# Optimization experiments

Hardware: AMD Instinct MI355X
Metric: run time of the kernel (lower is better)

Reference implementation:

```python
import jax, jax.numpy as jnp
import numpy as np

N = 50000
E = 1600000
NEG_SLOPE = 0.2
EPS = 1e-16


def gat_conv(x, src, dst, W, att_src, att_dst, bias):
    # x: [N, F_in]; W: [F_in, H*C]; att_*: [H, C]; bias: [H*C]
    H, C = att_src.shape
    h = (x @ W).reshape(-1, H, C)               # [N, H, C]
    a_src = jnp.sum(h * att_src[None], axis=-1)  # [N, H]
    a_dst = jnp.sum(h * att_dst[None], axis=-1)  # [N, H]
    e = a_src[src] + a_dst[dst]                  # [E, H]
    e = jnp.where(e > 0, e, NEG_SLOPE * e)       # leaky_relu
    # segment softmax over incoming edges of each destination node
    m = jax.ops.segment_max(e, dst, num_segments=N)          # [N, H]
    ex = jnp.exp(e - m[dst])                                  # [E, H]
    s = jax.ops.segment_sum(ex, dst, num_segments=N)          # [N, H]
    alpha = ex / (s[dst] + EPS)                               # [E, H]
    out = jax.ops.segment_sum(h[src] * alpha[:, :, None], dst, num_segments=N)  # [N, H, C]
    return out.reshape(-1, H * C) + bias


def setup_inputs() -> dict:
    key = jax.random.key(0)
    ks = jax.random.split(key, 12)
    x = jax.random.normal(ks[0], (N, 128), dtype=jnp.float32)
    edge_index = jax.random.randint(ks[1], (2, E), 0, N, dtype=jnp.int64)
    W1 = jax.random.normal(ks[2], (128, 128), dtype=jnp.float32) * 0.1
    att_src1 = jax.random.normal(ks[3], (4, 32), dtype=jnp.float32) * 0.1
    att_dst1 = jax.random.normal(ks[4], (4, 32), dtype=jnp.float32) * 0.1
    bias1 = jax.random.normal(ks[5], (128,), dtype=jnp.float32) * 0.1
    W2 = jax.random.normal(ks[6], (128, 64), dtype=jnp.float32) * 0.1
    att_src2 = jax.random.normal(ks[7], (1, 64), dtype=jnp.float32) * 0.1
    att_dst2 = jax.random.normal(ks[8], (1, 64), dtype=jnp.float32) * 0.1
    bias2 = jax.random.normal(ks[9], (64,), dtype=jnp.float32) * 0.1
    return {"x": x, "edge_index": edge_index, "W1": W1, "att_src1": att_src1,
            "att_dst1": att_dst1, "bias1": bias1, "W2": W2, "att_src2": att_src2,
            "att_dst2": att_dst2, "bias2": bias2}


def reference(x, edge_index, W1, att_src1, att_dst1, bias1, W2, att_src2, att_dst2, bias2):
    # GATConv adds self loops by default
    loops = jnp.arange(N, dtype=edge_index.dtype)
    src = jnp.concatenate([edge_index[0], loops])
    dst = jnp.concatenate([edge_index[1], loops])
    # eval mode: dropouts are identity
    h = gat_conv(x, src, dst, W1, att_src1, att_dst1, bias1)
    h = jax.nn.elu(h)
    out = gat_conv(h, src, dst, W2, att_src2, att_dst2, bias2)
    return out
```

## Files before the change

### kernel.cpp

```cpp
#include <hip/hip_runtime.h>
#include <hip/hip_fp16.h>
#include <math.h>


#define NB_BUCKETS 256
#define BCAP 16384

typedef _Float16 half8 __attribute__((ext_vector_type(8)));
typedef float    floatx4 __attribute__((ext_vector_type(4)));

__device__ __forceinline__ unsigned short f2h_bits(float f) {
    return __half_as_ushort(__float2half(f));
}
__device__ __forceinline__ float h2f_lo(unsigned int u) {
    return __half2float(__ushort_as_half((unsigned short)(u & 0xFFFFu)));
}
__device__ __forceinline__ float h2f_hi(unsigned int u) {
    return __half2float(__ushort_as_half((unsigned short)(u >> 16)));
}

__global__ __launch_bounds__(256) void splitA_kernel(const int* __restrict__ eidx,
        unsigned int* __restrict__ tmp, int* __restrict__ coarse_fill,
        int E, int etot, int nb)
{
    __shared__ int hist[NB_BUCKETS];
    __shared__ int gb[NB_BUCKETS];
    __shared__ int cnt2[NB_BUCKETS];
    int t = threadIdx.x;
    if (t < nb) { hist[t] = 0; cnt2[t] = 0; }
    __syncthreads();

    unsigned int val[16];
    int bkt[16];
    int base = blockIdx.x * 4096;
    #pragma unroll
    for (int i = 0; i < 16; i++) {
        int idx = base + i * 256 + t;
        if (idx < etot) {
            unsigned int s, d;
            if (idx < E) { s = (unsigned int)eidx[idx]; d = (unsigned int)eidx[E + idx]; }
            else         { s = (unsigned int)(idx - E); d = s; }
            val[i] = (d << 16) | s;
            bkt[i] = (int)(d >> 8);
            atomicAdd(&hist[bkt[i]], 1);
        } else {
            bkt[i] = -1;
        }
    }
    __syncthreads();
    if (t < nb) {
        int n = hist[t];
        gb[t] = (n > 0) ? atomicAdd(&coarse_fill[t], n) : 0;
    }
    __syncthreads();
    #pragma unroll
    for (int i = 0; i < 16; i++) {
        if (bkt[i] >= 0) {
            int loc = atomicAdd(&cnt2[bkt[i]], 1);
            tmp[(size_t)bkt[i] * BCAP + gb[bkt[i]] + loc] = val[i];
        }
    }
}

__global__ __launch_bounds__(256) void scanB_kernel(const int* __restrict__ coarse_fill,
        int* __restrict__ bucket_base, int nb, int N_, int etot, int* __restrict__ rowp)
{
    __shared__ int sd[256];
    int t = threadIdx.x;
    int c = (t < nb) ? coarse_fill[t] : 0;
    sd[t] = c;
    __syncthreads();
    for (int off = 1; off < 256; off <<= 1) {
        int y = (t >= off) ? sd[t - off] : 0;
        __syncthreads();
        sd[t] += y;
        __syncthreads();
    }
    if (t < nb) bucket_base[t] = sd[t] - c;
    if (t == 0) rowp[N_] = etot;
}

__global__ __launch_bounds__(1024) void passB_kernel(const unsigned int* __restrict__ tmp,
        const int* __restrict__ coarse_fill, const int* __restrict__ bucket_base,
        int* __restrict__ col, int* __restrict__ rowp, int N_)
{
    __shared__ int hist2[256];
    __shared__ int scn[256];
    __shared__ int off2[256];
    int b = blockIdx.x;
    int t = threadIdx.x;
    int n = coarse_fill[b];
    int base = bucket_base[b];
    const unsigned int* seg = tmp + (size_t)b * BCAP;

    if (t < 256) hist2[t] = 0;
    __syncthreads();
    for (int i = t; i < n; i += 1024) {
        unsigned int v = seg[i];
        atomicAdd(&hist2[(v >> 16) & 255], 1);
    }
    __syncthreads();
    int myc = (t < 256) ? hist2[t] : 0;
    if (t < 256) scn[t] = myc;
    __syncthreads();
    for (int off = 1; off < 256; off <<= 1) {
        int y = 0;
        if (t < 256 && t >= off) y = scn[t - off];
        __syncthreads();
        if (t < 256) scn[t] += y;
        __syncthreads();
    }
    if (t < 256) {
        int excl = scn[t] - myc;
        off2[t] = excl;
        int node = b * 256 + t;
        if (node <= N_) rowp[node] = base + excl;
    }
    __syncthreads();
    for (int i = t; i < n; i += 1024) {
        unsigned int v = seg[i];
        int bin = (v >> 16) & 255;
        int loc = atomicAdd(&off2[bin], 1);
        col[base + loc] = (int)(v & 0xFFFFu);
    }
}

template<int NT, int H, bool AF16>
__global__ __launch_bounds__(256) void gemm_attn_kernel(
        const void* __restrict__ Xv, const float* __restrict__ W,
        const float* __restrict__ att_s, const float* __restrict__ att_d,
        unsigned short* __restrict__ Hf16, float* __restrict__ as_,
        float* __restrict__ ad_, int M)
{
    constexpr int D = NT * 16;
    constexpr int C = D / H;
    __shared__ _Float16 Bs[NT * 4 * 64 * 8];

    int t = threadIdx.x;
    for (int idx = t; idx < 128 * D; idx += 256) {
        int k = idx / D;
        int n = idx - k * D;
        int nt = n >> 4, ks = k >> 5;
        int lane = (((k >> 3) & 3) << 4) | (n & 15);
        int j = k & 7;
        Bs[(((nt * 4 + ks) * 64 + lane) << 3) + j] = (_Float16)W[idx];
    }
    __syncthreads();

    int lane = t & 63;
    int wv = t >> 6;
    int quad = lane >> 4, colL = lane & 15;
    int row0 = blockIdx.x * 64 + wv * 16;

    int arow = row0 + colL; if (arow > M - 1) arow = M - 1;
    half8 afrag[4];
    if constexpr (AF16) {
        const unsigned short* Xh = (const unsigned short*)Xv;
        #pragma unroll
        for (int ks = 0; ks < 4; ks++)
            afrag[ks] = *(const half8*)(const void*)(Xh + (size_t)arow * 128 + ks * 32 + quad * 8);
    } else {
        const float* Xf = (const float*)Xv;
        #pragma unroll
        for (int ks = 0; ks < 4; ks++) {
            const float* pa = Xf + (size_t)arow * 128 + ks * 32 + quad * 8;
            float4 a0 = *(const float4*)pa;
            float4 a1 = *(const float4*)(pa + 4);
            half8 f;
            f[0] = (_Float16)a0.x; f[1] = (_Float16)a0.y;
            f[2] = (_Float16)a0.z; f[3] = (_Float16)a0.w;
            f[4] = (_Float16)a1.x; f[5] = (_Float16)a1.y;
            f[6] = (_Float16)a1.z; f[7] = (_Float16)a1.w;
            afrag[ks] = f;
        }
    }

    floatx4 acc[NT];
    #pragma unroll
    for (int nt = 0; nt < NT; nt++) {
        floatx4 c = {0.f, 0.f, 0.f, 0.f};
        #pragma unroll
        for (int ks = 0; ks < 4; ks++) {
            half8 b = *(half8*)(void*)&Bs[(((nt * 4 + ks) * 64 + lane) << 3)];
            c = __builtin_amdgcn_mfma_f32_16x16x32_f16(afrag[ks], b, c, 0, 0, 0);
        }
        acc[nt] = c;
    }

    float atts[NT], attd[NT];
    #pragma unroll
    for (int nt = 0; nt < NT; nt++) {
        int ch = nt * 16 + colL;
        atts[nt] = att_s[ch];
        attd[nt] = att_d[ch];
    }
    float ps[H][4], pd[H][4];
    #pragma unroll
    for (int h = 0; h < H; h++)
        #pragma unroll
        for (int r = 0; r < 4; r++) { ps[h][r] = 0.f; pd[h][r] = 0.f; }
    #pragma unroll
    for (int nt = 0; nt < NT; nt++) {
        int h = (nt * 16) / C;
        #pragma unroll
        for (int r = 0; r < 4; r++) {
            ps[h][r] += acc[nt][r] * atts[nt];
            pd[h][r] += acc[nt][r] * attd[nt];
        }
    }
    #pragma unroll
    for (int h = 0; h < H; h++)
        #pragma unroll
        for (int r = 0; r < 4; r++)
            #pragma unroll
            for (int off = 1; off < 16; off <<= 1) {
                ps[h][r] += __shfl_xor(ps[h][r], off);
                pd[h][r] += __shfl_xor(pd[h][r], off);
            }
    if (colL < H) {
        #pragma unroll
        for (int r = 0; r < 4; r++) {
            int row = row0 + quad * 4 + r;
            if (row < M) {
                float vs, vd;
                if constexpr (H == 4) {
                    vs = colL == 0 ? ps[0][r] : colL == 1 ? ps[1][r] : colL == 2 ? ps[2][r] : ps[3][r];
                    vd = colL == 0 ? pd[0][r] : colL == 1 ? pd[1][r] : colL == 2 ? pd[2][r] : pd[3][r];
                } else {
                    vs = ps[0][r]; vd = pd[0][r];
                }
                as_[(size_t)row * H + colL] = vs;
                ad_[(size_t)row * H + colL] = vd;
            }
        }
    }

    #pragma unroll
    for (int r = 0; r < 4; r++) {
        int row = row0 + quad * 4 + r;
        if (row < M) {
            #pragma unroll
            for (int nt = 0; nt < NT; nt++)
                Hf16[(size_t)row * D + nt * 16 + colL] = f2h_bits(acc[nt][r]);
        }
    }
}

template<int H, int C, bool ELU_, bool OUTF16>
__global__ __launch_bounds__(256) void aggregate_fused(
        const int* __restrict__ row_ptr, const int* __restrict__ col_src,
        const unsigned short* __restrict__ payload, const float* __restrict__ asv,
        const float* __restrict__ adv, const float* __restrict__ bias,
        void* __restrict__ outv, int nnodes)
{
    constexpr int D = H * C;
    constexpr int CPL = 8;
    constexpr int LPE = D / CPL;
    constexpr int EPI = 64 / LPE;
    __shared__ float2 exs[4][H][65];
    int wave = threadIdx.x >> 6, lane = threadIdx.x & 63;
    int node = blockIdx.x * 4 + wave;
    if (node >= nnodes) return;
    int start = row_ptr[node];
    int deg   = row_ptr[node + 1] - start;
    int li  = lane & (LPE - 1);
    int sub = lane / LPE;
    int myh = (li * CPL) / C;
    int lane_off = li * 16;

    float adh[H];
    #pragma unroll
    for (int h = 0; h < H; h++) adh[h] = adv[(size_t)node * H + h];

    float m[H];
    #pragma unroll
    for (int h = 0; h < H; h++) m[h] = -3.0e38f;
    float acc[CPL];
    #pragma unroll
    for (int k = 0; k < CPL; k++) acc[k] = 0.f;
    float sacc = 0.f;
    const char* pb = (const char*)payload;

    for (int c0 = 0; c0 < deg; c0 += 64) {
        int cnt = deg - c0; if (cnt > 64) cnt = 64;
        int idx = c0 + lane;
        int svec = 0;
        float e[H];
        if (idx < deg) {
            svec = col_src[start + idx];
            if constexpr (H == 4) {
                float4 av = *(const float4*)(asv + (size_t)svec * 4);
                float t0 = av.x + adh[0], t1 = av.y + adh[1];
                float t2 = av.z + adh[2], t3 = av.w + adh[3];
                e[0] = fmaxf(t0, 0.2f * t0); e[1] = fmaxf(t1, 0.2f * t1);
                e[2] = fmaxf(t2, 0.2f * t2); e[3] = fmaxf(t3, 0.2f * t3);
            } else {
                float tt = asv[svec] + adh[0];
                e[0] = fmaxf(tt, 0.2f * tt);
            }
        } else {
            #pragma unroll
            for (int h = 0; h < H; h++) e[h] = -3.0e38f;
        }
        float nm[H];
        #pragma unroll
        for (int h = 0; h < H; h++) {
            float v = e[h];
            #pragma unroll
            for (int off = 32; off >= 1; off >>= 1)
                v = fmaxf(v, __shfl_xor(v, off));
            nm[h] = fmaxf(m[h], v);
        }
        float sc = __expf(m[myh] - nm[myh]);
        sacc *= sc;
        #pragma unroll
        for (int k = 0; k < CPL; k++) acc[k] *= sc;
        #pragma unroll
        for (int h = 0; h < H; h++) m[h] = nm[h];

        unsigned int boff = (unsigned int)svec * (unsigned int)(D * 2);
        float boff_f = __uint_as_float(boff);
        #pragma unroll
        for (int h = 0; h < H; h++) {
            float ex = (idx < deg) ? __expf(e[h] - m[h]) : 0.f;
            exs[wave][h][lane] = make_float2(ex, boff_f);
        }

        int iters = (cnt + EPI - 1) / EPI;
        #pragma unroll 2
        for (int it = 0; it < iters; it++) {
            int el = it * EPI + sub;
            float2 v = exs[wave][myh][el];
            float exj = v.x;
            unsigned int off = __float_as_uint(v.y);
            uint4 hv = *(const uint4*)(const void*)(pb + off + lane_off);
            sacc += exj;
            acc[0] = fmaf(h2f_lo(hv.x), exj, acc[0]);
            acc[1] = fmaf(h2f_hi(hv.x), exj, acc[1]);
            acc[2] = fmaf(h2f_lo(hv.y), exj, acc[2]);
            acc[3] = fmaf(h2f_hi(hv.y), exj, acc[3]);
            acc[4] = fmaf(h2f_lo(hv.z), exj, acc[4]);
            acc[5] = fmaf(h2f_hi(hv.z), exj, acc[5]);
            acc[6] = fmaf(h2f_lo(hv.w), exj, acc[6]);
            acc[7] = fmaf(h2f_hi(hv.w), exj, acc[7]);
        }
    }

    #pragma unroll
    for (int off = LPE; off < 64; off <<= 1) {
        sacc += __shfl_xor(sacc, off);
        #pragma unroll
        for (int k = 0; k < CPL; k++) acc[k] += __shfl_xor(acc[k], off);
    }
    if (sub == 0) {
        float inv = 1.f / (sacc + 1e-16f);
        int ch = li * CPL;
        float r[CPL];
        #pragma unroll
        for (int k = 0; k < CPL; k++) {
            r[k] = acc[k] * inv + bias[ch + k];
            if (ELU_) r[k] = r[k] > 0.f ? r[k] : (__expf(r[k]) - 1.f);
        }
        if constexpr (OUTF16) {
            unsigned short* o = (unsigned short*)outv;
            unsigned int w0 = (unsigned int)f2h_bits(r[0]) | ((unsigned int)f2h_bits(r[1]) << 16);
            unsigned int w1 = (unsigned int)f2h_bits(r[2]) | ((unsigned int)f2h_bits(r[3]) << 16);
            unsigned int w2 = (unsigned int)f2h_bits(r[4]) | ((unsigned int)f2h_bits(r[5]) << 16);
            unsigned int w3 = (unsigned int)f2h_bits(r[6]) | ((unsigned int)f2h_bits(r[7]) << 16);
            uint4 q = { w0, w1, w2, w3 };
            *(uint4*)(void*)(o + (size_t)node * D + ch) = q;
        } else {
            float* o = (float*)outv;
            float4 w0 = { r[0], r[1], r[2], r[3] };
            float4 w1 = { r[4], r[5], r[6], r[7] };
            *(float4*)(o + (size_t)node * D + ch) = w0;
            *(float4*)(o + (size_t)node * D + ch + 4) = w1;
        }
    }
}

extern "C" void kernel_launch(void* const* d_in, const int* in_sizes, int n_in,
                              void* d_out, int out_size, void* d_ws, size_t ws_size,
                              hipStream_t stream)
{
    const float* x        = (const float*)d_in[0];
    const int*   eidx     = (const int*)  d_in[1];
    const float* W1       = (const float*)d_in[2];
    const float* att_src1 = (const float*)d_in[3];
    const float* att_dst1 = (const float*)d_in[4];
    const float* bias1    = (const float*)d_in[5];
    const float* W2       = (const float*)d_in[6];
    const float* att_src2 = (const float*)d_in[7];
    const float* att_dst2 = (const float*)d_in[8];
    const float* bias2    = (const float*)d_in[9];
    float* out = (float*)d_out;

    const int N_ = in_sizes[0] / 128;
    const int E_ = in_sizes[1] / 2;
    const int ET = E_ + N_;
    const int NB = (N_ + 255) / 256;

    char* p = (char*)d_ws;
    auto alloc = [&](size_t bytes) {
        void* r = (void*)p;
        p += ((bytes + 255) / 256) * 256;
        return r;
    };
    int* rowp  = (int*)alloc((size_t)(N_ + 1) * 4);
    int* cfill = (int*)alloc((size_t)NB_BUCKETS * 4);
    int* bbase = (int*)alloc((size_t)NB_BUCKETS * 4);
    int* colidx = (int*)alloc((size_t)ET * 4);
    unsigned int*   tmp   = (unsigned int*)alloc((size_t)NB_BUCKETS * BCAP * 4);
    unsigned short* h1f16 = (unsigned short*)tmp;
    unsigned short* hx16  = (unsigned short*)alloc((size_t)N_ * 128 * 2);
    unsigned short* h2f16 = (unsigned short*)alloc((size_t)N_ * 64 * 2);
    float* as1 = (float*)alloc((size_t)N_ * 4 * 4);
    float* ad1 = (float*)alloc((size_t)N_ * 4 * 4);
    float* as2 = (float*)alloc((size_t)N_ * 4);
    float* ad2 = (float*)alloc((size_t)N_ * 4);
    (void)ws_size; (void)n_in; (void)out_size;

    hipMemsetAsync(cfill, 0, (size_t)NB_BUCKETS * 4, stream);
    splitA_kernel<<<(ET + 4095) / 4096, 256, 0, stream>>>(eidx, tmp, cfill, E_, ET, NB);
    scanB_kernel<<<1, 256, 0, stream>>>(cfill, bbase, NB, N_, ET, rowp);
    passB_kernel<<<NB, 1024, 0, stream>>>(tmp, cfill, bbase, colidx, rowp, N_);

    gemm_attn_kernel<8, 4, false><<<(N_ + 63) / 64, 256, 0, stream>>>(
        x, W1, att_src1, att_dst1, h1f16, as1, ad1, N_);
    aggregate_fused<4, 32, true, true><<<(N_ + 3) / 4, 256, 0, stream>>>(
        rowp, colidx, h1f16, as1, ad1, bias1, hx16, N_);

    gemm_attn_kernel<4, 1, true><<<(N_ + 63) / 64, 256, 0, stream>>>(
        hx16, W2, att_src2, att_dst2, h2f16, as2, ad2, N_);
    aggregate_fused<1, 64, false, false><<<(N_ + 3) / 4, 256, 0, stream>>>(
        rowp, colidx, h2f16, as2, ad2, bias2, out, N_);
}
```

Before: 245.5 us.

## Merge CSR build with first GEMM, fold scan into passB, split aggregation channels

Runs the first GEMM+attention blocks and the edge-bucketing blocks in one launch so they share the device. The single-block scan kernel is folded into passB, where each block recomputes the bucket prefix sum itself. The aggregation kernels now split channels into two halves across separate blocks, which doubles block count and halves per-wave payload width but recomputes softmax weights twice per edge. h1 gets its own buffer instead of aliasing the tmp buffer, because the tmp buckets are now written concurrently.

After: 271.3 us. +10.5%, slower.

```diff
diff --git a/kernel.cpp b/kernel.cpp
--- a/kernel.cpp
+++ b/kernel.cpp
@@ -19,7 +19,7 @@
     return __half2float(__ushort_as_half((unsigned short)(u >> 16)));
 }
 
-__global__ __launch_bounds__(256) void splitA_kernel(const int* __restrict__ eidx,
+__device__ void splitA_body(int bx, const int* __restrict__ eidx,
         unsigned int* __restrict__ tmp, int* __restrict__ coarse_fill,
         int E, int etot, int nb)
 {
@@ -32,7 +32,7 @@
 
     unsigned int val[16];
     int bkt[16];
-    int base = blockIdx.x * 4096;
+    int base = bx * 4096;
     #pragma unroll
     for (int i = 0; i < 16; i++) {
         int idx = base + i * 256 + t;
@@ -62,71 +62,8 @@
     }
 }
 
-__global__ __launch_bounds__(256) void scanB_kernel(const int* __restrict__ coarse_fill,
-        int* __restrict__ bucket_base, int nb, int N_, int etot, int* __restrict__ rowp)
-{
-    __shared__ int sd[256];
-    int t = threadIdx.x;
-    int c = (t < nb) ? coarse_fill[t] : 0;
-    sd[t] = c;
-    __syncthreads();
-    for (int off = 1; off < 256; off <<= 1) {
-        int y = (t >= off) ? sd[t - off] : 0;
-        __syncthreads();
-        sd[t] += y;
-        __syncthreads();
-    }
-    if (t < nb) bucket_base[t] = sd[t] - c;
-    if (t == 0) rowp[N_] = etot;
-}
-
-__global__ __launch_bounds__(1024) void passB_kernel(const unsigned int* __restrict__ tmp,
-        const int* __restrict__ coarse_fill, const int* __restrict__ bucket_base,
-        int* __restrict__ col, int* __restrict__ rowp, int N_)
-{
-    __shared__ int hist2[256];
-    __shared__ int scn[256];
-    __shared__ int off2[256];
-    int b = blockIdx.x;
-    int t = threadIdx.x;
-    int n = coarse_fill[b];
-    int base = bucket_base[b];
-    const unsigned int* seg = tmp + (size_t)b * BCAP;
-
-    if (t < 256) hist2[t] = 0;
-    __syncthreads();
-    for (int i = t; i < n; i += 1024) {
-        unsigned int v = seg[i];
-        atomicAdd(&hist2[(v >> 16) & 255], 1);
-    }
-    __syncthreads();
-    int myc = (t < 256) ? hist2[t] : 0;
-    if (t < 256) scn[t] = myc;
-    __syncthreads();
-    for (int off = 1; off < 256; off <<= 1) {
-        int y = 0;
-        if (t < 256 && t >= off) y = scn[t - off];
-        __syncthreads();
-        if (t < 256) scn[t] += y;
-        __syncthreads();
-    }
-    if (t < 256) {
-        int excl = scn[t] - myc;
-        off2[t] = excl;
-        int node = b * 256 + t;
-        if (node <= N_) rowp[node] = base + excl;
-    }
-    __syncthreads();
-    for (int i = t; i < n; i += 1024) {
-        unsigned int v = seg[i];
-        int bin = (v >> 16) & 255;
-        int loc = atomicAdd(&off2[bin], 1);
-        col[base + loc] = (int)(v & 0xFFFFu);
-    }
-}
-
 template<int NT, int H, bool AF16>
-__global__ __launch_bounds__(256) void gemm_attn_kernel(
+__device__ void gemm_attn_body(int bx,
         const void* __restrict__ Xv, const float* __restrict__ W,
         const float* __restrict__ att_s, const float* __restrict__ att_d,
         unsigned short* __restrict__ Hf16, float* __restrict__ as_,
@@ -150,7 +87,7 @@
     int lane = t & 63;
     int wv = t >> 6;
     int quad = lane >> 4, colL = lane & 15;
-    int row0 = blockIdx.x * 64 + wv * 16;
+    int row0 = bx * 64 + wv * 16;
 
     int arow = row0 + colL; if (arow > M - 1) arow = M - 1;
     half8 afrag[4];
@@ -246,27 +183,113 @@
     }
 }
 
+__global__ __launch_bounds__(256) void build_and_gemm1_kernel(
+        const int* __restrict__ eidx, unsigned int* __restrict__ tmp,
+        int* __restrict__ cfill, int E, int etot, int nb,
+        const float* __restrict__ x, const float* __restrict__ W1,
+        const float* __restrict__ att_s, const float* __restrict__ att_d,
+        unsigned short* __restrict__ h1f16, float* __restrict__ as1,
+        float* __restrict__ ad1, int M, int nbG)
+{
+    if ((int)blockIdx.x < nbG)
+        gemm_attn_body<8, 4, false>((int)blockIdx.x, x, W1, att_s, att_d,
+                                    h1f16, as1, ad1, M);
+    else
+        splitA_body((int)blockIdx.x - nbG, eidx, tmp, cfill, E, etot, nb);
+}
+
+__global__ __launch_bounds__(256) void gemm_attn2_kernel(
+        const void* __restrict__ Xv, const float* __restrict__ W,
+        const float* __restrict__ att_s, const float* __restrict__ att_d,
+        unsigned short* __restrict__ Hf16, float* __restrict__ as_,
+        float* __restrict__ ad_, int M)
+{
+    gemm_attn_body<4, 1, true>((int)blockIdx.x, Xv, W, att_s, att_d, Hf16, as_, ad_, M);
+}
+
+__global__ __launch_bounds__(1024) void passB_kernel(const unsigned int* __restrict__ tmp,
+        const int* __restrict__ cfill, int* __restrict__ col,
+        int* __restrict__ rowp, int N_, int nb, int etot)
+{
+    __shared__ int sd[256];
+    __shared__ int hist2[256];
+    __shared__ int scn[256];
+    __shared__ int off2[256];
+    int b = blockIdx.x;
+    int t = threadIdx.x;
+
+    int cf = 0;
+    if (t < 256) { cf = (t < nb) ? cfill[t] : 0; sd[t] = cf; }
+    __syncthreads();
+    for (int off = 1; off < 256; off <<= 1) {
+        int y = 0;
+        if (t < 256 && t >= off) y = sd[t - off];
+        __syncthreads();
+        if (t < 256) sd[t] += y;
+        __syncthreads();
+    }
+    int base = sd[b] - cfill[b];
+    int n = cfill[b];
+    const unsigned int* seg = tmp + (size_t)b * BCAP;
+
+    if (t < 256) hist2[t] = 0;
+    __syncthreads();
+    for (int i = t; i < n; i += 1024) {
+        unsigned int v = seg[i];
+        atomicAdd(&hist2[(v >> 16) & 255], 1);
+    }
+    __syncthreads();
+    int myc = (t < 256) ? hist2[t] : 0;
+    if (t < 256) scn[t] = myc;
+    __syncthreads();
+    for (int off = 1; off < 256; off <<= 1) {
+        int y = 0;
+        if (t < 256 && t >= off) y = scn[t - off];
+        __syncthreads();
+        if (t < 256) scn[t] += y;
+        __syncthreads();
+    }
+    if (t < 256) {
+        int excl = scn[t] - myc;
+        off2[t] = excl;
+        int node = b * 256 + t;
+        if (node <= N_) rowp[node] = base + excl;
+        if (node == N_) rowp[N_] = etot;
+    }
+    __syncthreads();
+    for (int i = t; i < n; i += 1024) {
+        unsigned int v = seg[i];
+        int bin = (v >> 16) & 255;
+        int loc = atomicAdd(&off2[bin], 1);
+        col[base + loc] = (int)(v & 0xFFFFu);
+    }
+}
+
 template<int H, int C, bool ELU_, bool OUTF16>
-__global__ __launch_bounds__(256) void aggregate_fused(
+__global__ __launch_bounds__(256) void aggregate_split(
         const int* __restrict__ row_ptr, const int* __restrict__ col_src,
         const unsigned short* __restrict__ payload, const float* __restrict__ asv,
         const float* __restrict__ adv, const float* __restrict__ bias,
-        void* __restrict__ outv, int nnodes)
+        void* __restrict__ outv, int nnodes, int nbh)
 {
     constexpr int D = H * C;
+    constexpr int HSPAN = D / 2;
     constexpr int CPL = 8;
-    constexpr int LPE = D / CPL;
+    constexpr int LPE = HSPAN / CPL;
     constexpr int EPI = 64 / LPE;
     __shared__ float2 exs[4][H][65];
+    int half = ((int)blockIdx.x >= nbh) ? 1 : 0;
+    int nodeblk = (int)blockIdx.x - half * nbh;
     int wave = threadIdx.x >> 6, lane = threadIdx.x & 63;
-    int node = blockIdx.x * 4 + wave;
+    int node = nodeblk * 4 + wave;
     if (node >= nnodes) return;
+    int ch0 = half * HSPAN;
     int start = row_ptr[node];
     int deg   = row_ptr[node + 1] - start;
     int li  = lane & (LPE - 1);
     int sub = lane / LPE;
-    int myh = (li * CPL) / C;
-    int lane_off = li * 16;
+    int myh = (ch0 + li * CPL) / C;
+    int lane_off = ch0 * 2 + li * 16;
 
     float adh[H];
     #pragma unroll
@@ -354,7 +377,7 @@
     }
     if (sub == 0) {
         float inv = 1.f / (sacc + 1e-16f);
-        int ch = li * CPL;
+        int ch = ch0 + li * CPL;
         float r[CPL];
         #pragma unroll
         for (int k = 0; k < CPL; k++) {
@@ -408,10 +431,9 @@
     };
     int* rowp  = (int*)alloc((size_t)(N_ + 1) * 4);
     int* cfill = (int*)alloc((size_t)NB_BUCKETS * 4);
-    int* bbase = (int*)alloc((size_t)NB_BUCKETS * 4);
     int* colidx = (int*)alloc((size_t)ET * 4);
     unsigned int*   tmp   = (unsigned int*)alloc((size_t)NB_BUCKETS * BCAP * 4);
-    unsigned short* h1f16 = (unsigned short*)tmp;
+    unsigned short* h1f16 = (unsigned short*)alloc((size_t)N_ * 128 * 2);
     unsigned short* hx16  = (unsigned short*)alloc((size_t)N_ * 128 * 2);
     unsigned short* h2f16 = (unsigned short*)alloc((size_t)N_ * 64 * 2);
     float* as1 = (float*)alloc((size_t)N_ * 4 * 4);
@@ -420,18 +442,19 @@
     float* ad2 = (float*)alloc((size_t)N_ * 4);
     (void)ws_size; (void)n_in; (void)out_size;
 
+    const int nbh = (N_ + 3) / 4;
+    const int nbG = (N_ + 63) / 64;
+    const int nbA = (ET + 4095) / 4096;
+
     hipMemsetAsync(cfill, 0, (size_t)NB_BUCKETS * 4, stream);
-    splitA_kernel<<<(ET + 4095) / 4096, 256, 0, stream>>>(eidx, tmp, cfill, E_, ET, NB);
-    scanB_kernel<<<1, 256, 0, stream>>>(cfill, bbase, NB, N_, ET, rowp);
-    passB_kernel<<<NB, 1024, 0, stream>>>(tmp, cfill, bbase, colidx, rowp, N_);
-
-    gemm_attn_kernel<8, 4, false><<<(N_ + 63) / 64, 256, 0, stream>>>(
-        x, W1, att_src1, att_dst1, h1f16, as1, ad1, N_);
-    aggregate_fused<4, 32, true, true><<<(N_ + 3) / 4, 256, 0, stream>>>(
-        rowp, colidx, h1f16, as1, ad1, bias1, hx16, N_);
-
-    gemm_attn_kernel<4, 1, true><<<(N_ + 63) / 64, 256, 0, stream>>>(
+    build_and_gemm1_kernel<<<nbG + nbA, 256, 0, stream>>>(
+        eidx, tmp, cfill, E_, ET, NB,
+        x, W1, att_src1, att_dst1, h1f16, as1, ad1, N_, nbG);
+    passB_kernel<<<NB, 1024, 0, stream>>>(tmp, cfill, colidx, rowp, N_, NB, ET);
+    aggregate_split<4, 32, true, true><<<2 * nbh, 256, 0, stream>>>(
+        rowp, colidx, h1f16, as1, ad1, bias1, hx16, N_, nbh);
+    gemm_attn2_kernel<<<nbG, 256, 0, stream>>>(
         hx16, W2, att_src2, att_dst2, h2f16, as2, ad2, N_);
-    aggregate_fused<1, 64, false, false><<<(N_ + 3) / 4, 256, 0, stream>>>(
-        rowp, colidx, h2f16, as2, ad2, bias2, out, N_);
-}
+    aggregate_split<1, 64, false, false><<<2 * nbh, 256, 0, stream>>>(
+        rowp, colidx, h2f16, as2, ad2, bias2, out, N_, nbh);
+}
```
